# Optimization experiments

Hardware: AMD Instinct MI355X
Metric: run time of the kernel (lower is better)

Reference implementation:

```python
import jax, jax.numpy as jnp
import numpy as np

N_NODES = 50000
N_EDGES = 1600000
IN_DIM = 128
OUT_DIM = 16
N_HEADS = 8


def setup_inputs() -> dict:
    key = jax.random.key(0)
    ks = jax.random.split(key, 9)
    s = 1.0 / np.sqrt(IN_DIM)
    return {
        "h": jax.random.normal(ks[0], (N_NODES, IN_DIM), jnp.float32),
        "Wq": jax.random.normal(ks[1], (IN_DIM, OUT_DIM * N_HEADS), jnp.float32) * s,
        "bq": jax.random.normal(ks[2], (OUT_DIM * N_HEADS,), jnp.float32) * 0.01,
        "Wk": jax.random.normal(ks[3], (IN_DIM, OUT_DIM * N_HEADS), jnp.float32) * s,
        "bk": jax.random.normal(ks[4], (OUT_DIM * N_HEADS,), jnp.float32) * 0.01,
        "Wv": jax.random.normal(ks[5], (IN_DIM, OUT_DIM * N_HEADS), jnp.float32) * s,
        "bv": jax.random.normal(ks[6], (OUT_DIM * N_HEADS,), jnp.float32) * 0.01,
        "src": jax.random.randint(ks[7], (N_EDGES,), 0, N_NODES, jnp.int32),
        "dst": jax.random.randint(ks[8], (N_EDGES,), 0, N_NODES, jnp.int32),
    }


def reference(h, Wq, bq, Wk, bk, Wv, bv, src, dst):
    n_nodes = h.shape[0]
    # node-wise Q/K/V projections -> [N, H, D]
    Q = (h @ Wq + bq).reshape(n_nodes, N_HEADS, OUT_DIM)
    K = (h @ Wk + bk).reshape(n_nodes, N_HEADS, OUT_DIM)
    V = (h @ Wv + bv).reshape(n_nodes, N_HEADS, OUT_DIM)
    # edge-wise score: (K[src] * Q[dst]).sum(-1), scaled-exp with clamp
    score = jnp.sum(K[src] * Q[dst], axis=-1)  # [E, H]
    score = jnp.exp(jnp.clip(score / np.sqrt(OUT_DIM), -5.0, 5.0))
    # scatter-sum weighted values and normalizers to dst nodes
    msg = V[src] * score[:, :, None]  # [E, H, D]
    wV = jax.ops.segment_sum(msg, dst, num_segments=n_nodes)  # [N, H, D]
    z = jax.ops.segment_sum(score, dst, num_segments=n_nodes)  # [N, H]
    return wV / (z[:, :, None] + 1e-6)
```

## Files before the change

### kernel.cpp

```cpp
#include <hip/hip_runtime.h>
#include <hip/hip_bf16.h>
#include <cstddef>

#define N_NODES 50000
#define N_EDGES 1600000
#define IN_DIM 128
#define OUT_DIM 16
#define N_HEADS 8
#define QKV_DIM 128
#define HS_STRIDE 136

#define SUBB 3125
#define SUBB_PAD 3136
#define BCAP 1024
#define BH_CHUNK 16384
#define BH_BLOCKS 98

typedef __hip_bfloat16 bf16;
typedef short bf16x8 __attribute__((ext_vector_type(8)));
typedef float f32x4  __attribute__((ext_vector_type(4)));

__device__ __forceinline__ float b2f(bf16 x) { return __bfloat162float(x); }

__device__ __forceinline__ float u16tof(unsigned int u) {
    unsigned int x = u << 16;
    float f;
    __builtin_memcpy(&f, &x, 4);
    return f;
}

__device__ __forceinline__ unsigned short f2bf(float v) {
    bf16 b = __float2bfloat16(v);
    unsigned short u;
    __builtin_memcpy(&u, &b, 2);
    return u;
}

__global__ __launch_bounds__(256) void init_kernel(int* __restrict__ p, int n) {
    int i = blockIdx.x * 256 + threadIdx.x;
    if (i < n) p[i] = 0;
}

__global__ __launch_bounds__(256) void detect_kernel(const unsigned short* __restrict__ hraw,
                                                     int* __restrict__ flag) {
    int t = threadIdx.x;
    int cnt = 0;
    for (int i = t; i < 8192; i += 256) {
        unsigned short u = hraw[i];
        int e = (u >> 7) & 0xFF;
        if (e == 0xFF || e > 0x85 || (e == 0 && (u & 0x7F) != 0)) cnt++;
    }
    atomicAdd(flag, cnt);
}

__global__ __launch_bounds__(256) void sentinel_kernel(unsigned short* __restrict__ out, int n) {
    int i = blockIdx.x * 256 + threadIdx.x;
    if (i < n) out[i] = 0x42C8;
}

__global__ __launch_bounds__(256) void prep_kernel(
    const void* __restrict__ Wqr, const void* __restrict__ bqr,
    const void* __restrict__ Wkr, const void* __restrict__ bkr,
    const void* __restrict__ Wvr, const void* __restrict__ bvr,
    const int* __restrict__ flag,
    unsigned short* __restrict__ Wfrag, float* __restrict__ bias_f)
{
    const bool f32 = (*flag > 100);
    int tid = blockIdx.x * 256 + threadIdx.x;

    if (tid < 384) {
        int mat = tid >> 7, c = tid & 127;
        const void* bp = (mat == 0) ? bqr : (mat == 1) ? bkr : bvr;
        bias_f[tid] = f32 ? ((const float*)bp)[c] : b2f(((const bf16*)bp)[c]);
    }
    if (tid >= 6144) return;

    int l  = tid & 63;
    int s  = (tid >> 6) & 3;
    int nt = tid >> 8;
    int n  = nt * 16 + (l & 15);
    int k0 = s * 32 + (l >> 4) * 8;
    int mat = n >> 7, c = n & 127;
    const void* Wp = (mat == 0) ? Wqr : (mat == 1) ? Wkr : Wvr;

    unsigned short v[8];
#pragma unroll
    for (int j = 0; j < 8; ++j) {
        int k = k0 + j;
        float w = f32 ? ((const float*)Wp)[k * QKV_DIM + c]
                      : b2f(((const bf16*)Wp)[k * QKV_DIM + c]);
        v[j] = f2bf(w);
    }
    ushort4* o = (ushort4*)(Wfrag + (size_t)tid * 8);
    o[0] = make_ushort4(v[0], v[1], v[2], v[3]);
    o[1] = make_ushort4(v[4], v[5], v[6], v[7]);
}

__global__ __launch_bounds__(256) void gemm_kernel(
    const void* __restrict__ hraw,
    const unsigned short* __restrict__ Wfrag, const float* __restrict__ bias_f,
    const int* __restrict__ flag,
    unsigned short* __restrict__ Qt, unsigned short* __restrict__ KVt)
{
    __shared__ __align__(16) unsigned short hs[64 * HS_STRIDE];

    const bool f32 = (*flag > 100);
    const int m0  = blockIdx.x * 64;
    const int tid = threadIdx.x;

#pragma unroll
    for (int it = 0; it < 8; ++it) {
        int idx = it * 1024 + tid * 4;
        int r = idx >> 7, k = idx & 127;
        int row = m0 + r;
        ushort4 w4 = make_ushort4(0, 0, 0, 0);
        if (row < N_NODES) {
            if (f32) {
                float4 v4 = ((const float4*)hraw)[(size_t)row * 32 + (k >> 2)];
                w4 = make_ushort4(f2bf(v4.x), f2bf(v4.y), f2bf(v4.z), f2bf(v4.w));
            } else {
                uint2 u = ((const uint2*)hraw)[(size_t)row * 32 + (k >> 2)];
                w4 = make_ushort4((unsigned short)(u.x & 0xffffu), (unsigned short)(u.x >> 16),
                                  (unsigned short)(u.y & 0xffffu), (unsigned short)(u.y >> 16));
            }
        }
        *(ushort4*)&hs[r * HS_STRIDE + k] = w4;
    }
    __syncthreads();

    const int lane = tid & 63;
    const int wave = tid >> 6;
    const int qd   = lane >> 4;
    const int ln15 = lane & 15;

    bf16x8 afr[4][4];
#pragma unroll
    for (int ms = 0; ms < 4; ++ms)
#pragma unroll
        for (int s = 0; s < 4; ++s)
            afr[ms][s] = *(const bf16x8*)&hs[(ms * 16 + ln15) * HS_STRIDE + s * 32 + qd * 8];

#pragma unroll
    for (int i = 0; i < 6; ++i) {
        const int nt  = wave + i * 4;
        const int col = nt * 16 + ln15;
        const float bs = bias_f[col];
        const int mat = col >> 7, c127 = col & 127;
        const int coff = (mat == 0) ? c127
                       : 8 * (c127 >> 2) + (c127 & 3) + ((mat == 2) ? 4 : 0);

        bf16x8 bfr[4];
#pragma unroll
        for (int s = 0; s < 4; ++s)
            bfr[s] = *(const bf16x8*)(Wfrag + ((size_t)(nt * 4 + s) * 64 + lane) * 8);

#pragma unroll
        for (int ms = 0; ms < 4; ++ms) {
            f32x4 acc = {0.f, 0.f, 0.f, 0.f};
#pragma unroll
            for (int s = 0; s < 4; ++s)
                acc = __builtin_amdgcn_mfma_f32_16x16x32_bf16(afr[ms][s], bfr[s], acc, 0, 0, 0);
#pragma unroll
            for (int r = 0; r < 4; ++r) {
                int row = m0 + ms * 16 + qd * 4 + r;
                if (row < N_NODES) {
                    unsigned short val = f2bf(acc[r] + bs);
                    if (mat == 0) Qt[row * 128 + coff] = val;
                    else          KVt[row * 256 + coff] = val;
                }
            }
        }
    }
}

__global__ __launch_bounds__(256) void scatter_kernel(const int* __restrict__ src,
                                                      const int* __restrict__ dst,
                                                      int* __restrict__ gcursor,
                                                      unsigned int* __restrict__ packed) {
    __shared__ int lcnt[SUBB];
    __shared__ int lbase[SUBB];
    int t = threadIdx.x;
    for (int i = t; i < SUBB; i += 256) lcnt[i] = 0;
    __syncthreads();
    int base = blockIdx.x * BH_CHUNK;
    for (int i = 0; i < 64; ++i) {
        int e = base + i * 256 + t;
        if (e < N_EDGES) atomicAdd(&lcnt[dst[e] >> 4], 1);
    }
    __syncthreads();
    for (int i = t; i < SUBB; i += 256) {
        int c = lcnt[i];
        lbase[i] = c ? atomicAdd(&gcursor[i], c) : 0;
        lcnt[i] = 0;
    }
    __syncthreads();
    for (int i = 0; i < 64; ++i) {
        int e = base + i * 256 + t;
        if (e < N_EDGES) {
            int d = dst[e];
            int b = d >> 4;
            int pos = lbase[b] + atomicAdd(&lcnt[b], 1);
            if (pos < BCAP)
                packed[b * BCAP + pos] = (unsigned int)src[e] | ((unsigned int)(d & 15) << 16);
        }
    }
}

__global__ __launch_bounds__(256) void bucket_agg_kernel(
    const unsigned short* __restrict__ Qt, const unsigned short* __restrict__ KVt,
    const unsigned int* __restrict__ packed, const int* __restrict__ gcursor,
    const int* __restrict__ flag, void* __restrict__ out)
{
    __shared__ unsigned int   lds_pk[BCAP];
    __shared__ unsigned short lds_src[BCAP];
    __shared__ int cnt16[16], base16[16], cur16[16];

    const int sb = blockIdx.x;
    const int t  = threadIdx.x;
    const int nb = min(gcursor[sb], BCAP);

    if (t < 16) { cnt16[t] = 0; cur16[t] = 0; }
    __syncthreads();

    for (int j = t; j < nb; j += 256) {
        unsigned int pk = packed[sb * BCAP + j];
        lds_pk[j] = pk;
        atomicAdd(&cnt16[(pk >> 16) & 15], 1);
    }
    __syncthreads();
    if (t == 0) {
        int acc = 0;
#pragma unroll
        for (int i = 0; i < 16; ++i) { base16[i] = acc; acc += cnt16[i]; }
    }
    __syncthreads();
    for (int j = t; j < nb; j += 256) {
        unsigned int pk = lds_pk[j];
        int dl = (pk >> 16) & 15;
        int pos = base16[dl] + atomicAdd(&cur16[dl], 1);
        lds_src[pos] = (unsigned short)(pk & 0xffffu);
    }
    __syncthreads();

    const int wave = t >> 6;
    const int lane = t & 63;
    const int half = lane >> 5;
    const int hl   = lane & 31;
    const uint4* KV4 = (const uint4*)KVt;
    const bool of32 = (*flag > 100);

    for (int dl = wave; dl < 16; dl += 4) {
        const int d = sb * 16 + dl;
        uint2 qw = ((const uint2*)Qt)[d * 32 + hl];
        const float q0 = u16tof(qw.x & 0xffffu), q1 = u16tof(qw.x >> 16);
        const float q2 = u16tof(qw.y & 0xffffu), q3 = u16tof(qw.y >> 16);
        const int off = base16[dl];
        const int n   = cnt16[dl];

        float a0 = 0.f, a1 = 0.f, a2 = 0.f, a3 = 0.f, zz = 0.f;

#define CONSUME(KV, SCMASK)                                                     \
        {                                                                       \
            float p = fmaf(u16tof((KV).x & 0xffffu), q0,                        \
                      fmaf(u16tof((KV).x >> 16), q1,                            \
                      fmaf(u16tof((KV).y & 0xffffu), q2,                        \
                           u16tof((KV).y >> 16) * q3)));                        \
            p += __shfl_xor(p, 1);                                              \
            p += __shfl_xor(p, 2);                                              \
            float sc = __expf(__builtin_amdgcn_fmed3f(p * 0.25f, -5.f, 5.f));   \
            sc *= (SCMASK);                                                     \
            a0 = fmaf(u16tof((KV).z & 0xffffu), sc, a0);                        \
            a1 = fmaf(u16tof((KV).z >> 16),     sc, a1);                        \
            a2 = fmaf(u16tof((KV).w & 0xffffu), sc, a2);                        \
            a3 = fmaf(u16tof((KV).w >> 16),     sc, a3);                        \
            zz += sc;                                                           \
        }

        int j = 0;
        for (; j + 8 <= n; j += 8) {
            int e[4];
#pragma unroll
            for (int u = 0; u < 4; ++u) e[u] = lds_src[off + j + 2 * u + half];
            uint4 kv[4];
#pragma unroll
            for (int u = 0; u < 4; ++u) kv[u] = KV4[e[u] * 32 + hl];
#pragma unroll
            for (int u = 0; u < 4; ++u) CONSUME(kv[u], 1.f)
        }
        for (; j + 2 <= n; j += 2) {
            int e = lds_src[off + j + half];
            uint4 kv = KV4[e * 32 + hl];
            CONSUME(kv, 1.f)
        }
        if (j < n) {
            int e = lds_src[off + j];
            uint4 kv = KV4[e * 32 + hl];
            CONSUME(kv, (half == 0) ? 1.f : 0.f)
        }
#undef CONSUME

        a0 += __shfl_xor(a0, 32);
        a1 += __shfl_xor(a1, 32);
        a2 += __shfl_xor(a2, 32);
        a3 += __shfl_xor(a3, 32);
        zz += __shfl_xor(zz, 32);

        const float inv = 1.f / (zz + 1e-6f);
        const float r0 = a0 * inv, r1 = a1 * inv, r2 = a2 * inv, r3 = a3 * inv;

        if (half == 0) {
            if (of32) {
                ((float4*)out)[d * 32 + hl] = make_float4(r0, r1, r2, r3);
            } else {
                unsigned int w0 = ((unsigned int)f2bf(r1) << 16) | f2bf(r0);
                unsigned int w1 = ((unsigned int)f2bf(r3) << 16) | f2bf(r2);
                ((uint2*)out)[d * 32 + hl] = make_uint2(w0, w1);
            }
        }
    }
}

extern "C" void kernel_launch(void* const* d_in, const int* in_sizes, int n_in,
                              void* d_out, int out_size, void* d_ws, size_t ws_size,
                              hipStream_t stream)
{
    const void* h  = d_in[0];
    const void* Wq = d_in[1];
    const void* bq = d_in[2];
    const void* Wk = d_in[3];
    const void* bk = d_in[4];
    const void* Wv = d_in[5];
    const void* bv = d_in[6];
    const int*  src = (const int*)d_in[7];
    const int*  dst = (const int*)d_in[8];

    const size_t NQ = (size_t)N_NODES * QKV_DIM;
    const size_t WFRAG_N = 24 * 4 * 64 * 8;

    const size_t need = 3 * NQ * 2 + WFRAG_N * 2 + 384 * 4
                      + ((size_t)SUBB_PAD + 16) * sizeof(int)
                      + (size_t)SUBB * BCAP * 4;

    if (ws_size < need) {
        sentinel_kernel<<<(out_size + 255) / 256, 256, 0, stream>>>((unsigned short*)d_out, out_size);
        return;
    }

    unsigned short* Qt  = (unsigned short*)d_ws;
    unsigned short* KVt = Qt + NQ;
    unsigned short* Wfrag = KVt + 2 * NQ;
    float* bias_f = (float*)(Wfrag + WFRAG_N);
    int* gcursor = (int*)(bias_f + 384);
    int* flag    = gcursor + SUBB_PAD;
    unsigned int* packed = (unsigned int*)(flag + 16);

    const int zero_n = SUBB_PAD + 16;
    init_kernel<<<(zero_n + 255) / 256, 256, 0, stream>>>(gcursor, zero_n);
    detect_kernel<<<1, 256, 0, stream>>>((const unsigned short*)h, flag);

    prep_kernel<<<24, 256, 0, stream>>>(Wq, bq, Wk, bk, Wv, bv, flag, Wfrag, bias_f);

    const int gemm_blocks = (N_NODES + 63) / 64;
    gemm_kernel<<<gemm_blocks, 256, 0, stream>>>(h, Wfrag, bias_f, flag, Qt, KVt);

    scatter_kernel<<<BH_BLOCKS, 256, 0, stream>>>(src, dst, gcursor, packed);

    bucket_agg_kernel<<<SUBB, 256, 0, stream>>>(Qt, KVt, packed, gcursor, flag, d_out);
}
```

Baseline: 309.1 us.

## Fuse init and detect kernels, stage GEMM output in LDS, deepen aggregation unroll

Merges the zero-init and dtype-detect launches into one kernel, using a block reduction that writes the flag directly instead of an atomic. The GEMM epilogue now stages its bf16 results in a larger shared buffer and writes Q and KV rows as coalesced 16-byte stores rather than scattered 2-byte stores. The aggregation kernel gains an occupancy hint and a 16-edge unrolled loop for more outstanding gathers. The trade-offs are higher LDS use per GEMM block, which may lower its occupancy, and more register pressure in the aggregation kernel.

```diff
diff --git a/kernel.cpp b/kernel.cpp
--- a/kernel.cpp
+++ b/kernel.cpp
@@ -9,6 +9,7 @@
 #define N_HEADS 8
 #define QKV_DIM 128
 #define HS_STRIDE 136
+#define OS_STRIDE 392
 
 #define SUBB 3125
 #define SUBB_PAD 3136
@@ -36,21 +37,30 @@
     return u;
 }
 
-__global__ __launch_bounds__(256) void init_kernel(int* __restrict__ p, int n) {
-    int i = blockIdx.x * 256 + threadIdx.x;
-    if (i < n) p[i] = 0;
-}
-
-__global__ __launch_bounds__(256) void detect_kernel(const unsigned short* __restrict__ hraw,
-                                                     int* __restrict__ flag) {
+__global__ __launch_bounds__(256) void init_detect_kernel(
+    int* __restrict__ p, int nz_words,
+    const unsigned short* __restrict__ hraw, int* __restrict__ flag, int nblocks)
+{
+    __shared__ int red[256];
     int t = threadIdx.x;
-    int cnt = 0;
-    for (int i = t; i < 8192; i += 256) {
-        unsigned short u = hraw[i];
-        int e = (u >> 7) & 0xFF;
-        if (e == 0xFF || e > 0x85 || (e == 0 && (u & 0x7F) != 0)) cnt++;
-    }
-    atomicAdd(flag, cnt);
+    if ((int)blockIdx.x == nblocks - 1) {
+        int cnt = 0;
+        for (int i = t; i < 8192; i += 256) {
+            unsigned short u = hraw[i];
+            int e = (u >> 7) & 0xFF;
+            if (e == 0xFF || e > 0x85 || (e == 0 && (u & 0x7F) != 0)) cnt++;
+        }
+        red[t] = cnt;
+        __syncthreads();
+        for (int s = 128; s > 0; s >>= 1) {
+            if (t < s) red[t] += red[t + s];
+            __syncthreads();
+        }
+        if (t == 0) *flag = red[0];
+    } else {
+        int i = blockIdx.x * 256 + t;
+        if (i < nz_words) p[i] = 0;
+    }
 }
 
 __global__ __launch_bounds__(256) void sentinel_kernel(unsigned short* __restrict__ out, int n) {
@@ -102,7 +112,7 @@
     const int* __restrict__ flag,
     unsigned short* __restrict__ Qt, unsigned short* __restrict__ KVt)
 {
-    __shared__ __align__(16) unsigned short hs[64 * HS_STRIDE];
+    __shared__ __align__(16) unsigned short smem[64 * OS_STRIDE];
 
     const bool f32 = (*flag > 100);
     const int m0  = blockIdx.x * 64;
@@ -124,7 +134,7 @@
                                   (unsigned short)(u.y & 0xffffu), (unsigned short)(u.y >> 16));
             }
         }
-        *(ushort4*)&hs[r * HS_STRIDE + k] = w4;
+        *(ushort4*)&smem[r * HS_STRIDE + k] = w4;
     }
     __syncthreads();
 
@@ -138,7 +148,9 @@
     for (int ms = 0; ms < 4; ++ms)
 #pragma unroll
         for (int s = 0; s < 4; ++s)
-            afr[ms][s] = *(const bf16x8*)&hs[(ms * 16 + ln15) * HS_STRIDE + s * 32 + qd * 8];
+            afr[ms][s] = *(const bf16x8*)&smem[(ms * 16 + ln15) * HS_STRIDE + s * 32 + qd * 8];
+
+    __syncthreads();
 
 #pragma unroll
     for (int i = 0; i < 6; ++i) {
@@ -146,8 +158,8 @@
         const int col = nt * 16 + ln15;
         const float bs = bias_f[col];
         const int mat = col >> 7, c127 = col & 127;
-        const int coff = (mat == 0) ? c127
-                       : 8 * (c127 >> 2) + (c127 & 3) + ((mat == 2) ? 4 : 0);
+        const int ocol = (mat == 0) ? c127
+                       : 128 + 8 * (c127 >> 2) + (c127 & 3) + ((mat == 2) ? 4 : 0);
 
         bf16x8 bfr[4];
 #pragma unroll
@@ -162,14 +174,24 @@
                 acc = __builtin_amdgcn_mfma_f32_16x16x32_bf16(afr[ms][s], bfr[s], acc, 0, 0, 0);
 #pragma unroll
             for (int r = 0; r < 4; ++r) {
-                int row = m0 + ms * 16 + qd * 4 + r;
-                if (row < N_NODES) {
-                    unsigned short val = f2bf(acc[r] + bs);
-                    if (mat == 0) Qt[row * 128 + coff] = val;
-                    else          KVt[row * 256 + coff] = val;
-                }
+                int rl = ms * 16 + qd * 4 + r;
+                smem[rl * OS_STRIDE + ocol] = f2bf(acc[r] + bs);
             }
         }
+    }
+    __syncthreads();
+
+    for (int q = tid; q < 1024; q += 256) {
+        int row = q >> 4, c = q & 15;
+        int grow = m0 + row;
+        if (grow < N_NODES)
+            ((uint4*)Qt)[grow * 16 + c] = *(const uint4*)&smem[row * OS_STRIDE + c * 8];
+    }
+    for (int q = tid; q < 2048; q += 256) {
+        int row = q >> 5, g = q & 31;
+        int grow = m0 + row;
+        if (grow < N_NODES)
+            ((uint4*)KVt)[grow * 32 + g] = *(const uint4*)&smem[row * OS_STRIDE + 128 + g * 8];
     }
 }
 
@@ -206,7 +228,7 @@
     }
 }
 
-__global__ __launch_bounds__(256) void bucket_agg_kernel(
+__global__ __launch_bounds__(256, 8) void bucket_agg_kernel(
     const unsigned short* __restrict__ Qt, const unsigned short* __restrict__ KVt,
     const unsigned int* __restrict__ packed, const int* __restrict__ gcursor,
     const int* __restrict__ flag, void* __restrict__ out)
@@ -277,7 +299,17 @@
         }
 
         int j = 0;
-        for (; j + 8 <= n; j += 8) {
+        for (; j + 16 <= n; j += 16) {
+            int e[8];
+#pragma unroll
+            for (int u = 0; u < 8; ++u) e[u] = lds_src[off + j + 2 * u + half];
+            uint4 kv[8];
+#pragma unroll
+            for (int u = 0; u < 8; ++u) kv[u] = KV4[e[u] * 32 + hl];
+#pragma unroll
+            for (int u = 0; u < 8; ++u) CONSUME(kv[u], 1.f)
+        }
+        if (j + 8 <= n) {
             int e[4];
 #pragma unroll
             for (int u = 0; u < 4; ++u) e[u] = lds_src[off + j + 2 * u + half];
@@ -286,6 +318,7 @@
             for (int u = 0; u < 4; ++u) kv[u] = KV4[e[u] * 32 + hl];
 #pragma unroll
             for (int u = 0; u < 4; ++u) CONSUME(kv[u], 1.f)
+            j += 8;
         }
         for (; j + 2 <= n; j += 2) {
             int e = lds_src[off + j + half];
@@ -354,9 +387,10 @@
     int* flag    = gcursor + SUBB_PAD;
     unsigned int* packed = (unsigned int*)(flag + 16);
 
-    const int zero_n = SUBB_PAD + 16;
-    init_kernel<<<(zero_n + 255) / 256, 256, 0, stream>>>(gcursor, zero_n);
-    detect_kernel<<<1, 256, 0, stream>>>((const unsigned short*)h, flag);
+    const int nz = SUBB_PAD;
+    const int id_blocks = (nz + 255) / 256 + 1;
+    init_detect_kernel<<<id_blocks, 256, 0, stream>>>(gcursor, nz,
+        (const unsigned short*)h, flag, id_blocks);
 
     prep_kernel<<<24, 256, 0, stream>>>(Wq, bq, Wk, bk, Wv, bv, flag, Wfrag, bias_f);
 
```

Measured after the change: 298.6 us. -3.4%, faster.
